# Kernel optimization log

Measured on AMD Instinct MI355X. Metric: run time of the kernel, lower is better.

## Reference

```python
import jax, jax.numpy as jnp
import numpy as np

N_NODES = 50000
N_EDGES = 1200000
N_GRAPHS = 1024
N_FEAT = 9
EMB = 64


def setup_inputs() -> dict:
    key = jax.random.key(0)
    ks = jax.random.split(key, 10)
    x = jax.random.normal(ks[0], (N_NODES, N_FEAT), dtype=jnp.float32)
    edge_index = jax.random.randint(ks[1], (2, N_EDGES), 0, N_NODES, dtype=jnp.int32)
    # sorted, gap-free graph assignment (every graph non-empty)
    batch_index = (jnp.arange(N_NODES, dtype=jnp.int32) * N_GRAPHS) // N_NODES
    batch_index = batch_index.astype(jnp.int32)

    def glorot(k, shape):
        lim = float(np.sqrt(6.0 / (shape[0] + shape[1])))
        return jax.random.uniform(k, shape, jnp.float32, -lim, lim)

    return {
        'x': x,
        'edge_index': edge_index,
        'batch_index': batch_index,
        'W0': glorot(ks[2], (N_FEAT, EMB)), 'b0': jnp.zeros((EMB,), jnp.float32),
        'W1': glorot(ks[3], (EMB, EMB)),   'b1': jnp.zeros((EMB,), jnp.float32),
        'W2': glorot(ks[4], (EMB, EMB)),   'b2': jnp.zeros((EMB,), jnp.float32),
        'W3': glorot(ks[5], (EMB, EMB)),   'b3': jnp.zeros((EMB,), jnp.float32),
        'Wout': glorot(ks[6], (2 * EMB, 1)), 'bout': jnp.zeros((1,), jnp.float32),
    }


def _gcn_conv(h_in, W, b, src, dst, edge_norm, self_norm, n_nodes):
    # h = X W ; out[i] = sum_{(j->i)} norm_e * h[j] + (1/deg_i) * h[i] + b
    h = h_in @ W
    msg = h[src] * edge_norm[:, None]                      # [E, emb]
    agg = jax.ops.segment_sum(msg, dst, num_segments=n_nodes)
    return agg + h * self_norm[:, None] + b


def reference(x, edge_index, batch_index, W0, b0, W1, b1, W2, b2, W3, b3, Wout, bout):
    src, dst = edge_index[0], edge_index[1]
    n_nodes = x.shape[0]
    # degree with self-loops (unit edge weights)
    deg = jax.ops.segment_sum(jnp.ones_like(src, dtype=x.dtype), dst,
                              num_segments=n_nodes) + 1.0
    dinv_sqrt = jax.lax.rsqrt(deg)
    edge_norm = dinv_sqrt[src] * dinv_sqrt[dst]            # [E]
    self_norm = 1.0 / deg                                  # [N]

    h = jnp.tanh(_gcn_conv(x, W0, b0, src, dst, edge_norm, self_norm, n_nodes))
    h = jnp.tanh(_gcn_conv(h, W1, b1, src, dst, edge_norm, self_norm, n_nodes))
    h = jnp.tanh(_gcn_conv(h, W2, b2, src, dst, edge_norm, self_norm, n_nodes))
    h = jnp.tanh(_gcn_conv(h, W3, b3, src, dst, edge_norm, self_norm, n_nodes))

    gmp = jax.ops.segment_max(h, batch_index, num_segments=N_GRAPHS)
    counts = jax.ops.segment_sum(jnp.ones((n_nodes,), h.dtype), batch_index,
                                 num_segments=N_GRAPHS)
    gap = jax.ops.segment_sum(h, batch_index, num_segments=N_GRAPHS) / counts[:, None]
    pooled = jnp.concatenate([gmp, gap], axis=1)           # [G, 2*emb]
    return pooled @ Wout + bout
```

## Files before the change

### kernel.cpp

```cpp
#include <hip/hip_runtime.h>

#define N_NODES  50000
#define N_EDGES  1200000
#define N_GRAPHS 1024
#define N_FEAT   9
#define EMB      64
#define SCAN_NB  ((N_NODES + 255) / 256)
#define KSPLIT   16


__global__ __launch_bounds__(256) void rank_kernel(const int* __restrict__ dst,
                                                   int* __restrict__ cntk,
                                                   int* __restrict__ rank, int ne) {
    int i = blockIdx.x * blockDim.x + threadIdx.x;
    if (i < ne) {
        int k = i & (KSPLIT - 1);
        rank[i] = atomicAdd(&cntk[k * N_NODES + dst[i]], 1);
    }
}

__global__ __launch_bounds__(256) void merge_kernel(int* __restrict__ cntk,
                                                    const float* __restrict__ x,
                                                    const int* __restrict__ batch,
                                                    int* __restrict__ cnt,
                                                    int* __restrict__ bsum,
                                                    float* __restrict__ dinv,
                                                    float* __restrict__ g0,
                                                    int* __restrict__ gstart, int n) {
    __shared__ int sw[4];
    int t = threadIdx.x;
    int i = blockIdx.x * 256 + t;
    int total = 0;
    if (i < n) {
        int s = 0;
#pragma unroll
        for (int k = 0; k < KSPLIT; ++k) {
            int c = cntk[k * N_NODES + i];
            cntk[k * N_NODES + i] = s;
            s += c;
        }
        total = s;
        cnt[i] = s;
        float d = (float)s + 1.0f;
        float dv = rsqrtf(d);
        dinv[i] = dv;
#pragma unroll
        for (int f = 0; f < N_FEAT; ++f)
            g0[i * N_FEAT + f] = dv * x[i * N_FEAT + f];
        int b = batch[i];
        if (i == 0 || batch[i - 1] != b) gstart[b] = i;
        if (i == 0) gstart[N_GRAPHS] = n;
    }
    int r = total;
#pragma unroll
    for (int off = 32; off; off >>= 1) r += __shfl_down(r, off, 64);
    if ((t & 63) == 0) sw[t >> 6] = r;
    __syncthreads();
    if (t == 0) bsum[blockIdx.x] = sw[0] + sw[1] + sw[2] + sw[3];
}

__global__ __launch_bounds__(256) void scanfill_kernel(const int* __restrict__ cnt,
                                                       const int* __restrict__ bsum,
                                                       int* __restrict__ rowp, int n) {
    __shared__ int sw[4];
    __shared__ int s_off;
    __shared__ int lds[256];
    int t = threadIdx.x;
    int p = (t < blockIdx.x) ? bsum[t] : 0;
#pragma unroll
    for (int off = 32; off; off >>= 1) p += __shfl_down(p, off, 64);
    if ((t & 63) == 0) sw[t >> 6] = p;
    __syncthreads();
    if (t == 0) s_off = sw[0] + sw[1] + sw[2] + sw[3];
    int i = blockIdx.x * 256 + t;
    int v = (i < n) ? cnt[i] : 0;
    lds[t] = v;
    __syncthreads();
    for (int off = 1; off < 256; off <<= 1) {
        int u = (t >= off) ? lds[t - off] : 0;
        __syncthreads();
        lds[t] += u;
        __syncthreads();
    }
    if (i < n) rowp[i] = s_off + lds[t] - v;
    if (i == 0) rowp[n] = N_EDGES;
}

__global__ __launch_bounds__(256) void fill2_kernel(const int* __restrict__ src,
                                                    const int* __restrict__ dst,
                                                    const int* __restrict__ rank,
                                                    const int* __restrict__ rowp,
                                                    const int* __restrict__ cntk,
                                                    int* __restrict__ csr, int ne) {
    int i = blockIdx.x * blockDim.x + threadIdx.x;
    if (i >= ne) return;
    int d = dst[i];
    int k = i & (KSPLIT - 1);
    csr[rowp[d] + cntk[k * N_NODES + d] + rank[i]] = src[i];
}


__global__ __launch_bounds__(256) void agg9_kernel(const float* __restrict__ g0,
                                                   const int* __restrict__ csr,
                                                   const int* __restrict__ rowp,
                                                   const float* __restrict__ dinv,
                                                   float* __restrict__ a, int n) {
    int wave = blockIdx.x * (blockDim.x >> 6) + (threadIdx.x >> 6);
    int lane = threadIdx.x & 63;
    if (wave >= n) return;
    int beg = rowp[wave], end = rowp[wave + 1];
    int slot = lane / 9;
    int f    = lane - slot * 9;
    float p = 0.0f;
    int e = beg;
    for (; e + 7 <= end; e += 7) {
        if (slot < 7) {
            int s = csr[e + slot];
            p += g0[s * N_FEAT + f];
        }
    }
    for (; e < end; ++e) {
        if (lane < N_FEAT) {
            int s = csr[e];
            p += g0[s * N_FEAT + lane];
        }
    }
    float tot = p;
#pragma unroll
    for (int s = 1; s < 7; ++s) {
        float t = __shfl(p, 9 * s + lane, 64);
        if (lane < N_FEAT) tot += t;
    }
    if (lane < N_FEAT)
        a[wave * N_FEAT + lane] = dinv[wave] * (tot + g0[wave * N_FEAT + lane]);
}


template <int K, bool PRESCALE>
__global__ __launch_bounds__(256) void gemm_tile_kernel(const float* __restrict__ in,
                                                        const float* __restrict__ W,
                                                        const float* __restrict__ b,
                                                        const float* __restrict__ dinv,
                                                        float* __restrict__ out, int n) {
    __shared__ float sIn[64 * (K + 1)];
    __shared__ float sW[K * EMB];
    int tid = threadIdx.x;
    int base = blockIdx.x * 64;
    for (int i = tid; i < K * EMB; i += 256) sW[i] = W[i];
    for (int i = tid; i < 64 * K; i += 256) {
        int r = i / K, c = i - r * K;
        int node = base + r;
        sIn[r * (K + 1) + c] = (node < n) ? in[(size_t)node * K + c] : 0.0f;
    }
    __syncthreads();
    int tx = tid & 15, ty = tid >> 4;
    int f0 = tx * 4, n0 = ty * 4;
    float acc[4][4];
#pragma unroll
    for (int i = 0; i < 4; ++i)
#pragma unroll
        for (int j = 0; j < 4; ++j) acc[i][j] = b[f0 + j];
#pragma unroll
    for (int k = 0; k < K; ++k) {
        float a0 = sIn[(n0 + 0) * (K + 1) + k];
        float a1 = sIn[(n0 + 1) * (K + 1) + k];
        float a2 = sIn[(n0 + 2) * (K + 1) + k];
        float a3 = sIn[(n0 + 3) * (K + 1) + k];
        float4 wv = *(const float4*)&sW[k * EMB + f0];
        acc[0][0] = fmaf(a0, wv.x, acc[0][0]);
        acc[0][1] = fmaf(a0, wv.y, acc[0][1]);
        acc[0][2] = fmaf(a0, wv.z, acc[0][2]);
        acc[0][3] = fmaf(a0, wv.w, acc[0][3]);
        acc[1][0] = fmaf(a1, wv.x, acc[1][0]);
        acc[1][1] = fmaf(a1, wv.y, acc[1][1]);
        acc[1][2] = fmaf(a1, wv.z, acc[1][2]);
        acc[1][3] = fmaf(a1, wv.w, acc[1][3]);
        acc[2][0] = fmaf(a2, wv.x, acc[2][0]);
        acc[2][1] = fmaf(a2, wv.y, acc[2][1]);
        acc[2][2] = fmaf(a2, wv.z, acc[2][2]);
        acc[2][3] = fmaf(a2, wv.w, acc[2][3]);
        acc[3][0] = fmaf(a3, wv.x, acc[3][0]);
        acc[3][1] = fmaf(a3, wv.y, acc[3][1]);
        acc[3][2] = fmaf(a3, wv.z, acc[3][2]);
        acc[3][3] = fmaf(a3, wv.w, acc[3][3]);
    }
#pragma unroll
    for (int i = 0; i < 4; ++i) {
        int node = base + n0 + i;
        if (node < n) {
            float dv = PRESCALE ? dinv[node] : 1.0f;
            float4 o;
            o.x = tanhf(acc[i][0]) * dv;
            o.y = tanhf(acc[i][1]) * dv;
            o.z = tanhf(acc[i][2]) * dv;
            o.w = tanhf(acc[i][3]) * dv;
            *(float4*)&out[(size_t)node * EMB + f0] = o;
        }
    }
}


template <bool PRESCALE>
__global__ __launch_bounds__(512) void fused_kernel(const float* __restrict__ gin,
                                                    const int* __restrict__ csr,
                                                    const int* __restrict__ rowp,
                                                    const float* __restrict__ dinv,
                                                    const float* __restrict__ W,
                                                    const float* __restrict__ b,
                                                    float* __restrict__ gout, int n) {
    __shared__ float sA[EMB * 65];
    __shared__ float sW[EMB * EMB];
    int tid = threadIdx.x;
    int base = blockIdx.x * 64;
    for (int i = tid; i < EMB * 16; i += 512)
        ((float4*)sW)[i] = ((const float4*)W)[i];
    int w = tid >> 6, lane = tid & 63;
    int slot = lane >> 5;
    int j = lane & 31;
    const float2* g2 = (const float2*)gin;
    for (int t = 0; t < 8; ++t) {
        int r = w + 8 * t;
        int node = base + r;
        float ax = 0.0f, ay = 0.0f;
        if (node < n) {
            int beg = rowp[node], end = rowp[node + 1];
            int e = beg;
            for (; e + 16 <= end; e += 16) {
                int s0 = csr[e + 0 + slot],  s1 = csr[e + 2 + slot];
                int s2 = csr[e + 4 + slot],  s3 = csr[e + 6 + slot];
                int s4 = csr[e + 8 + slot],  s5 = csr[e + 10 + slot];
                int s6 = csr[e + 12 + slot], s7 = csr[e + 14 + slot];
                float2 v0 = g2[(size_t)s0 * 32 + j], v1 = g2[(size_t)s1 * 32 + j];
                float2 v2 = g2[(size_t)s2 * 32 + j], v3 = g2[(size_t)s3 * 32 + j];
                float2 v4 = g2[(size_t)s4 * 32 + j], v5 = g2[(size_t)s5 * 32 + j];
                float2 v6 = g2[(size_t)s6 * 32 + j], v7 = g2[(size_t)s7 * 32 + j];
                ax += ((v0.x + v1.x) + (v2.x + v3.x)) + ((v4.x + v5.x) + (v6.x + v7.x));
                ay += ((v0.y + v1.y) + (v2.y + v3.y)) + ((v4.y + v5.y) + (v6.y + v7.y));
            }
            for (; e + 2 <= end; e += 2) {
                int s = csr[e + slot];
                float2 v = g2[(size_t)s * 32 + j];
                ax += v.x; ay += v.y;
            }
            if (e < end && slot == 0) {
                float2 v = g2[(size_t)csr[e] * 32 + j];
                ax += v.x; ay += v.y;
            }
        }
        ax += __shfl_down(ax, 32, 64);
        ay += __shfl_down(ay, 32, 64);
        if (slot == 0) {
            float ox = 0.0f, oy = 0.0f;
            if (node < n) {
                float2 self = g2[(size_t)node * 32 + j];
                float dv = dinv[node];
                ox = dv * (ax + self.x);
                oy = dv * (ay + self.y);
            }
            sA[(2 * j) * 65 + r]     = ox;
            sA[(2 * j + 1) * 65 + r] = oy;
        }
    }
    __syncthreads();
    int tx = tid & 15, ty = tid >> 4;
    int f0 = tx * 4, n0 = ty * 2;
    float4 bb = ((const float4*)b)[tx];
    float acc0[4] = {bb.x, bb.y, bb.z, bb.w};
    float acc1[4] = {bb.x, bb.y, bb.z, bb.w};
#pragma unroll 8
    for (int k = 0; k < EMB; ++k) {
        float a0 = sA[k * 65 + n0];
        float a1 = sA[k * 65 + n0 + 1];
        float4 wv = ((const float4*)sW)[k * 16 + tx];
        acc0[0] = fmaf(a0, wv.x, acc0[0]);
        acc0[1] = fmaf(a0, wv.y, acc0[1]);
        acc0[2] = fmaf(a0, wv.z, acc0[2]);
        acc0[3] = fmaf(a0, wv.w, acc0[3]);
        acc1[0] = fmaf(a1, wv.x, acc1[0]);
        acc1[1] = fmaf(a1, wv.y, acc1[1]);
        acc1[2] = fmaf(a1, wv.z, acc1[2]);
        acc1[3] = fmaf(a1, wv.w, acc1[3]);
    }
    int node0 = base + n0;
    if (node0 < n) {
        float dv = PRESCALE ? dinv[node0] : 1.0f;
        float4 o;
        o.x = tanhf(acc0[0]) * dv;
        o.y = tanhf(acc0[1]) * dv;
        o.z = tanhf(acc0[2]) * dv;
        o.w = tanhf(acc0[3]) * dv;
        *(float4*)&gout[(size_t)node0 * EMB + f0] = o;
    }
    if (node0 + 1 < n) {
        float dv = PRESCALE ? dinv[node0 + 1] : 1.0f;
        float4 o;
        o.x = tanhf(acc1[0]) * dv;
        o.y = tanhf(acc1[1]) * dv;
        o.z = tanhf(acc1[2]) * dv;
        o.w = tanhf(acc1[3]) * dv;
        *(float4*)&gout[(size_t)(node0 + 1) * EMB + f0] = o;
    }
}


__global__ __launch_bounds__(256) void pool_kernel(const float* __restrict__ h,
                                                   const int* __restrict__ gstart,
                                                   const float* __restrict__ Wout,
                                                   const float* __restrict__ bout,
                                                   float* __restrict__ out, int ng) {
    __shared__ float smx[4][EMB];
    __shared__ float ssm[4][EMB];
    int g = blockIdx.x;
    if (g >= ng) return;
    int w = threadIdx.x >> 6, lane = threadIdx.x & 63;
    int beg = gstart[g], end = gstart[g + 1];
    float mx = -3.0e38f, sm = 0.0f;
    for (int i = beg + w; i < end; i += 4) {
        float v = h[(size_t)i * EMB + lane];
        mx = fmaxf(mx, v);
        sm += v;
    }
    smx[w][lane] = mx;
    ssm[w][lane] = sm;
    __syncthreads();
    if (w == 0) {
        mx = fmaxf(fmaxf(smx[0][lane], smx[1][lane]), fmaxf(smx[2][lane], smx[3][lane]));
        sm = ssm[0][lane] + ssm[1][lane] + ssm[2][lane] + ssm[3][lane];
        float mean = sm / (float)(end - beg);
        float r = mx * Wout[lane] + mean * Wout[EMB + lane];
#pragma unroll
        for (int off = 32; off; off >>= 1) r += __shfl_down(r, off, 64);
        if (lane == 0) out[g] = r + bout[0];
    }
}


extern "C" void kernel_launch(void* const* d_in, const int* in_sizes, int n_in,
                              void* d_out, int out_size, void* d_ws, size_t ws_size,
                              hipStream_t stream) {
    const float* x     = (const float*)d_in[0];
    const int*   ei    = (const int*)d_in[1];
    const int*   batch = (const int*)d_in[2];
    const float* W0 = (const float*)d_in[3];
    const float* b0 = (const float*)d_in[4];
    const float* W1 = (const float*)d_in[5];
    const float* b1 = (const float*)d_in[6];
    const float* W2 = (const float*)d_in[7];
    const float* b2 = (const float*)d_in[8];
    const float* W3 = (const float*)d_in[9];
    const float* b3 = (const float*)d_in[10];
    const float* Wout = (const float*)d_in[11];
    const float* bout = (const float*)d_in[12];
    float* out = (float*)d_out;

    char* ws = (char*)d_ws;
    float* g_buf = (float*)ws;  ws += (size_t)N_NODES * EMB * 4;
    float* a_buf = (float*)ws;  ws += (size_t)N_NODES * EMB * 4;
    int*   csr   = (int*)ws;    ws += (size_t)N_EDGES * 4;
    int*   cnt   = (int*)ws;    ws += (size_t)N_NODES * 4;
    int*   rowp  = (int*)ws;    ws += (size_t)(N_NODES + 1) * 4;
    float* dinv  = (float*)ws;  ws += (size_t)N_NODES * 4;
    int*   gstart= (int*)ws;    ws += (size_t)(N_GRAPHS + 1) * 4;
    int*   bsum  = (int*)ws;    ws += (size_t)SCAN_NB * 4;
    int*   cntk  = (int*)a_buf;
    int*   rank  = (int*)a_buf + (size_t)KSPLIT * N_NODES;

    const int* srcp = ei;
    const int* dstp = ei + N_EDGES;

    hipMemsetAsync(cntk, 0, (size_t)KSPLIT * N_NODES * 4, stream);

    int ebl = (N_EDGES + 255) / 256;
    rank_kernel<<<ebl, 256, 0, stream>>>(dstp, cntk, rank, N_EDGES);
    merge_kernel<<<SCAN_NB, 256, 0, stream>>>(cntk, x, batch, cnt, bsum, dinv, g_buf,
                                              gstart, N_NODES);
    scanfill_kernel<<<SCAN_NB, 256, 0, stream>>>(cnt, bsum, rowp, N_NODES);
    fill2_kernel<<<ebl, 256, 0, stream>>>(srcp, dstp, rank, rowp, cntk, csr, N_EDGES);

    int wbl = (N_NODES + 3) / 4;
    int gbl = (N_NODES + 63) / 64;

    agg9_kernel<<<wbl, 256, 0, stream>>>(g_buf, csr, rowp, dinv, a_buf, N_NODES);
    gemm_tile_kernel<N_FEAT, true><<<gbl, 256, 0, stream>>>(a_buf, W0, b0, dinv,
                                                            g_buf, N_NODES);
    fused_kernel<true><<<gbl, 512, 0, stream>>>(g_buf, csr, rowp, dinv, W1, b1,
                                                a_buf, N_NODES);
    fused_kernel<true><<<gbl, 512, 0, stream>>>(a_buf, csr, rowp, dinv, W2, b2,
                                                g_buf, N_NODES);
    fused_kernel<false><<<gbl, 512, 0, stream>>>(g_buf, csr, rowp, dinv, W3, b3,
                                                 a_buf, N_NODES);

    pool_kernel<<<N_GRAPHS, 256, 0, stream>>>(a_buf, gstart, Wout, bout, out, N_GRAPHS);
}
```

Baseline: 381.4 us.

## Use float4 gathers with 4 edge slots and 32-node tiles in fused GCN kernel

The fused aggregate+GEMM kernel now gathers neighbor rows as float4, with 16 lanes per row and four edge slots per wavefront instead of float2 with two slots, then reduces the slots with two shuffle steps. The block tile shrinks from 64 to 32 nodes, which doubles the grid and halves shared memory per block. Each thread in the GEMM stage then computes one node instead of two. The intent is wider memory transactions, more parallel edges in flight and more blocks per CU for the gather-bound layers. The cost is extra shuffles, less W reuse per block, and the 16 KB W tile being loaded twice as often.

```diff
diff --git a/kernel.cpp b/kernel.cpp
--- a/kernel.cpp
+++ b/kernel.cpp
@@ -208,97 +208,96 @@
                                                     const float* __restrict__ W,
                                                     const float* __restrict__ b,
                                                     float* __restrict__ gout, int n) {
-    __shared__ float sA[EMB * 65];
+    __shared__ float sA[EMB * 33];
     __shared__ float sW[EMB * EMB];
     int tid = threadIdx.x;
-    int base = blockIdx.x * 64;
+    int base = blockIdx.x * 32;
     for (int i = tid; i < EMB * 16; i += 512)
         ((float4*)sW)[i] = ((const float4*)W)[i];
     int w = tid >> 6, lane = tid & 63;
-    int slot = lane >> 5;
-    int j = lane & 31;
-    const float2* g2 = (const float2*)gin;
-    for (int t = 0; t < 8; ++t) {
+    int slot = lane >> 4;
+    int j = lane & 15;
+    const float4* g4 = (const float4*)gin;
+#pragma unroll
+    for (int t = 0; t < 4; ++t) {
         int r = w + 8 * t;
         int node = base + r;
-        float ax = 0.0f, ay = 0.0f;
+        float4 acc = {0.0f, 0.0f, 0.0f, 0.0f};
         if (node < n) {
             int beg = rowp[node], end = rowp[node + 1];
             int e = beg;
             for (; e + 16 <= end; e += 16) {
-                int s0 = csr[e + 0 + slot],  s1 = csr[e + 2 + slot];
-                int s2 = csr[e + 4 + slot],  s3 = csr[e + 6 + slot];
-                int s4 = csr[e + 8 + slot],  s5 = csr[e + 10 + slot];
-                int s6 = csr[e + 12 + slot], s7 = csr[e + 14 + slot];
-                float2 v0 = g2[(size_t)s0 * 32 + j], v1 = g2[(size_t)s1 * 32 + j];
-                float2 v2 = g2[(size_t)s2 * 32 + j], v3 = g2[(size_t)s3 * 32 + j];
-                float2 v4 = g2[(size_t)s4 * 32 + j], v5 = g2[(size_t)s5 * 32 + j];
-                float2 v6 = g2[(size_t)s6 * 32 + j], v7 = g2[(size_t)s7 * 32 + j];
-                ax += ((v0.x + v1.x) + (v2.x + v3.x)) + ((v4.x + v5.x) + (v6.x + v7.x));
-                ay += ((v0.y + v1.y) + (v2.y + v3.y)) + ((v4.y + v5.y) + (v6.y + v7.y));
+                int s0 = csr[e + slot];
+                int s1 = csr[e + 4 + slot];
+                int s2 = csr[e + 8 + slot];
+                int s3 = csr[e + 12 + slot];
+                float4 v0 = g4[(size_t)s0 * 16 + j];
+                float4 v1 = g4[(size_t)s1 * 16 + j];
+                float4 v2 = g4[(size_t)s2 * 16 + j];
+                float4 v3 = g4[(size_t)s3 * 16 + j];
+                acc.x += (v0.x + v1.x) + (v2.x + v3.x);
+                acc.y += (v0.y + v1.y) + (v2.y + v3.y);
+                acc.z += (v0.z + v1.z) + (v2.z + v3.z);
+                acc.w += (v0.w + v1.w) + (v2.w + v3.w);
             }
-            for (; e + 2 <= end; e += 2) {
+            for (; e + 4 <= end; e += 4) {
                 int s = csr[e + slot];
-                float2 v = g2[(size_t)s * 32 + j];
-                ax += v.x; ay += v.y;
+                float4 v = g4[(size_t)s * 16 + j];
+                acc.x += v.x; acc.y += v.y; acc.z += v.z; acc.w += v.w;
             }
-            if (e < end && slot == 0) {
-                float2 v = g2[(size_t)csr[e] * 32 + j];
-                ax += v.x; ay += v.y;
+            if (e + slot < end) {
+                int s = csr[e + slot];
+                float4 v = g4[(size_t)s * 16 + j];
+                acc.x += v.x; acc.y += v.y; acc.z += v.z; acc.w += v.w;
             }
         }
-        ax += __shfl_down(ax, 32, 64);
-        ay += __shfl_down(ay, 32, 64);
+        acc.x += __shfl_down(acc.x, 32, 64);
+        acc.y += __shfl_down(acc.y, 32, 64);
+        acc.z += __shfl_down(acc.z, 32, 64);
+        acc.w += __shfl_down(acc.w, 32, 64);
+        acc.x += __shfl_down(acc.x, 16, 64);
+        acc.y += __shfl_down(acc.y, 16, 64);
+        acc.z += __shfl_down(acc.z, 16, 64);
+        acc.w += __shfl_down(acc.w, 16, 64);
         if (slot == 0) {
-            float ox = 0.0f, oy = 0.0f;
+            float ox = 0.0f, oy = 0.0f, oz = 0.0f, ow = 0.0f;
             if (node < n) {
-                float2 self = g2[(size_t)node * 32 + j];
+                float4 self = g4[(size_t)node * 16 + j];
                 float dv = dinv[node];
-                ox = dv * (ax + self.x);
-                oy = dv * (ay + self.y);
+                ox = dv * (acc.x + self.x);
+                oy = dv * (acc.y + self.y);
+                oz = dv * (acc.z + self.z);
+                ow = dv * (acc.w + self.w);
             }
-            sA[(2 * j) * 65 + r]     = ox;
-            sA[(2 * j + 1) * 65 + r] = oy;
+            sA[(4 * j + 0) * 33 + r] = ox;
+            sA[(4 * j + 1) * 33 + r] = oy;
+            sA[(4 * j + 2) * 33 + r] = oz;
+            sA[(4 * j + 3) * 33 + r] = ow;
         }
     }
     __syncthreads();
     int tx = tid & 15, ty = tid >> 4;
-    int f0 = tx * 4, n0 = ty * 2;
+    int f0 = tx * 4;
     float4 bb = ((const float4*)b)[tx];
-    float acc0[4] = {bb.x, bb.y, bb.z, bb.w};
-    float acc1[4] = {bb.x, bb.y, bb.z, bb.w};
+    float acc0 = bb.x, acc1 = bb.y, acc2 = bb.z, acc3 = bb.w;
 #pragma unroll 8
     for (int k = 0; k < EMB; ++k) {
-        float a0 = sA[k * 65 + n0];
-        float a1 = sA[k * 65 + n0 + 1];
+        float a0 = sA[k * 33 + ty];
         float4 wv = ((const float4*)sW)[k * 16 + tx];
-        acc0[0] = fmaf(a0, wv.x, acc0[0]);
-        acc0[1] = fmaf(a0, wv.y, acc0[1]);
-        acc0[2] = fmaf(a0, wv.z, acc0[2]);
-        acc0[3] = fmaf(a0, wv.w, acc0[3]);
-        acc1[0] = fmaf(a1, wv.x, acc1[0]);
-        acc1[1] = fmaf(a1, wv.y, acc1[1]);
-        acc1[2] = fmaf(a1, wv.z, acc1[2]);
-        acc1[3] = fmaf(a1, wv.w, acc1[3]);
-    }
-    int node0 = base + n0;
+        acc0 = fmaf(a0, wv.x, acc0);
+        acc1 = fmaf(a0, wv.y, acc1);
+        acc2 = fmaf(a0, wv.z, acc2);
+        acc3 = fmaf(a0, wv.w, acc3);
+    }
+    int node0 = base + ty;
     if (node0 < n) {
         float dv = PRESCALE ? dinv[node0] : 1.0f;
         float4 o;
-        o.x = tanhf(acc0[0]) * dv;
-        o.y = tanhf(acc0[1]) * dv;
-        o.z = tanhf(acc0[2]) * dv;
-        o.w = tanhf(acc0[3]) * dv;
+        o.x = tanhf(acc0) * dv;
+        o.y = tanhf(acc1) * dv;
+        o.z = tanhf(acc2) * dv;
+        o.w = tanhf(acc3) * dv;
         *(float4*)&gout[(size_t)node0 * EMB + f0] = o;
-    }
-    if (node0 + 1 < n) {
-        float dv = PRESCALE ? dinv[node0 + 1] : 1.0f;
-        float4 o;
-        o.x = tanhf(acc1[0]) * dv;
-        o.y = tanhf(acc1[1]) * dv;
-        o.z = tanhf(acc1[2]) * dv;
-        o.w = tanhf(acc1[3]) * dv;
-        *(float4*)&gout[(size_t)(node0 + 1) * EMB + f0] = o;
     }
 }
 
@@ -379,15 +378,16 @@
 
     int wbl = (N_NODES + 3) / 4;
     int gbl = (N_NODES + 63) / 64;
+    int fbl = (N_NODES + 31) / 32;
 
     agg9_kernel<<<wbl, 256, 0, stream>>>(g_buf, csr, rowp, dinv, a_buf, N_NODES);
     gemm_tile_kernel<N_FEAT, true><<<gbl, 256, 0, stream>>>(a_buf, W0, b0, dinv,
                                                             g_buf, N_NODES);
-    fused_kernel<true><<<gbl, 512, 0, stream>>>(g_buf, csr, rowp, dinv, W1, b1,
+    fused_kernel<true><<<fbl, 512, 0, stream>>>(g_buf, csr, rowp, dinv, W1, b1,
                                                 a_buf, N_NODES);
-    fused_kernel<true><<<gbl, 512, 0, stream>>>(a_buf, csr, rowp, dinv, W2, b2,
+    fused_kernel<true><<<fbl, 512, 0, stream>>>(a_buf, csr, rowp, dinv, W2, b2,
                                                 g_buf, N_NODES);
-    fused_kernel<false><<<gbl, 512, 0, stream>>>(g_buf, csr, rowp, dinv, W3, b3,
+    fused_kernel<false><<<fbl, 512, 0, stream>>>(g_buf, csr, rowp, dinv, W3, b3,
                                                  a_buf, N_NODES);
 
     pool_kernel<<<N_GRAPHS, 256, 0, stream>>>(a_buf, gstart, Wout, bout, out, N_GRAPHS);
```

Result: faster. 358.6 us (-6.0%).
